# Kernel tuning notes

Hardware: AMD Instinct MI355X
Metric: run time of the kernel (lower is better)

## Reference

```python
import jax, jax.numpy as jnp
import numpy as np

P_TOKENS = 200  # num_prompt_tokens
N_HEADS = 4


def setup_inputs() -> dict:
    key = jax.random.key(0)
    ks = jax.random.split(key, 6)
    B, N, C = 64, 1224, 1024
    D = 256  # bottleneck / down_size
    s = 0.02
    return {
        "x": jax.random.normal(ks[0], (B, N, C), dtype=jnp.float32),
        "down_W": jax.random.normal(ks[1], (D, C), dtype=jnp.float32) * s,
        "down_b": jnp.zeros((D,), jnp.float32),
        "up_W": jax.random.normal(ks[2], (C, D), dtype=jnp.float32) * s,
        "up_b": jnp.zeros((C,), jnp.float32),
        "in_proj_W": jax.random.normal(ks[3], (3 * D, D), dtype=jnp.float32) * s,
        "in_proj_b": jnp.zeros((3 * D,), jnp.float32),
        "out_proj_W": jax.random.normal(ks[4], (D, D), dtype=jnp.float32) * s,
        "out_proj_b": jnp.zeros((D,), jnp.float32),
        "gate": jnp.float32(1.0),
    }


def _forward(x, down_W, down_b, up_W, up_b, in_proj_W, in_proj_b,
             out_proj_W, out_proj_b, gate):
    B, N, C = x.shape
    E = down_W.shape[0]
    hd = E // N_HEADS
    # down projection + exact GELU (torch nn.GELU default)
    down = jax.nn.gelu(x @ down_W.T + down_b, approximate=False)  # [B,N,E]
    prompt = down[:, :P_TOKENS, :]   # [B,P,E]
    tok = down[:, P_TOKENS:, :]      # [B,T,E]
    # --- nn.MultiheadAttention(prompt, prompt, prompt) ---
    qkv = prompt @ in_proj_W.T + in_proj_b            # [B,P,3E]
    q, k, v = jnp.split(qkv, 3, axis=-1)
    def heads(t):
        return t.reshape(B, P_TOKENS, N_HEADS, hd)
    q, k, v = heads(q), heads(k), heads(v)
    attn = jnp.einsum('bqhd,bkhd->bhqk', q, k) / jnp.sqrt(jnp.float32(hd))
    attn = jax.nn.softmax(attn, axis=-1)
    sa = jnp.einsum('bhqk,bkhd->bqhd', attn, v).reshape(B, P_TOKENS, E)
    sa = sa @ out_proj_W.T + out_proj_b               # [B,P,E]
    # --- manual cross attention prompt -> tokens ---
    scale = jnp.float32(E) ** -0.5
    cross = jax.nn.softmax(jnp.einsum('bpe,bte->bpt', sa, tok) * scale, axis=-1)
    prompt_out = jnp.einsum('bpt,bte->bpe', cross, tok)  # [B,P,E]
    combined = jnp.concatenate([prompt_out, tok], axis=1)  # [B,N,E]
    up = combined @ up_W.T + up_b                          # [B,N,C]
    return gate * up


def reference(x, down_W, down_b, up_W, up_b, in_proj_W, in_proj_b,
              out_proj_W, out_proj_b, gate):
    return _forward(x, down_W, down_b, up_W, up_b, in_proj_W, in_proj_b,
                    out_proj_W, out_proj_b, gate)
```

## Files before the change

### kernel.cpp

```cpp
#include <hip/hip_runtime.h>
#include <math.h>

#define BB 64
#define NN 1224
#define CC 1024
#define DD 256
#define PP 200
#define TT 1024
#define HH 4
#define HDD 64

typedef __attribute__((ext_vector_type(8))) short bf16x8;
typedef __attribute__((ext_vector_type(4))) float f32x4;
typedef unsigned short u16;
typedef unsigned long long u64;

__device__ __forceinline__ u16 f2bf(float f) {
  union { float f; unsigned int u; } v; v.f = f;
  unsigned int r = v.u + 0x7FFF + ((v.u >> 16) & 1);
  return (u16)(r >> 16);
}
__device__ __forceinline__ float bf2f(u16 h) {
  union { unsigned int u; float f; } v; v.u = ((unsigned int)h) << 16;
  return v.f;
}
__device__ __forceinline__ unsigned int pk2(float a, float b) {
  return (unsigned int)f2bf(a) | ((unsigned int)f2bf(b) << 16);
}
__device__ __forceinline__ void gload16(const void* g, void* l) {
  __builtin_amdgcn_global_load_lds(
      (const __attribute__((address_space(1))) void*)g,
      (__attribute__((address_space(3))) void*)l, 16, 0, 0);
}

static const size_t SZ_DOWN = (size_t)BB * NN * DD * 2;
static const size_t SZ_TOKT = (size_t)BB * DD * TT * 2;
static const size_t SZ_Q    = (size_t)BB * HH * PP * HDD * 2;
static const size_t SZ_SCORES = (size_t)BB * PP * TT * 2;

static const size_t B_DOWN   = 0;
static const size_t B_TOKT   = B_DOWN + SZ_DOWN;
static const size_t B_POOL   = B_TOKT + SZ_TOKT;
static const size_t B_QB     = B_POOL;
static const size_t B_KB     = B_QB + SZ_Q;
static const size_t B_VB     = B_KB + SZ_Q;
static const size_t B_SA     = B_VB + SZ_Q;
static const size_t B_SA2    = B_SA + SZ_Q;
static const size_t B_PBF    = B_POOL;
static const size_t B_POUTBF = B_SA2;
static const size_t B_SCORES = B_SA2 + SZ_Q;
static const size_t B_W      = B_SCORES + SZ_SCORES * 2;
static const size_t B_WD     = B_W;
static const size_t B_WU     = B_WD + 524288;
static const size_t B_WIP    = B_WU + 524288;
static const size_t B_WOP    = B_WIP + 393216;

#define GEMM_VARS \
  const int tid = threadIdx.x; \
  const int lane = tid & 63, wave = tid >> 6; \
  const int wm = wave >> 2, wn = wave & 3; \
  f32x4 acc[4][4] = {};

#define MFMA_STEP(Ab, Bb) \
  _Pragma("unroll") \
  for (int kk = 0; kk < 64; kk += 32) { \
    bf16x8 af[4], bfr[4]; \
    _Pragma("unroll") \
    for (int mi = 0; mi < 4; ++mi) { \
      const int R = wm * 64 + mi * 16 + (lane & 15); \
      const int byt = (R * 128 + (kk + (lane >> 4) * 8) * 2) ^ ((R & 7) << 4); \
      af[mi] = *(const bf16x8*)((const char*)Ab + byt); \
    } \
    _Pragma("unroll") \
    for (int ni = 0; ni < 4; ++ni) { \
      const int R = wn * 64 + ni * 16 + (lane & 15); \
      const int byt = (R * 128 + (kk + (lane >> 4) * 8) * 2) ^ ((R & 7) << 4); \
      bfr[ni] = *(const bf16x8*)((const char*)Bb + byt); \
    } \
    _Pragma("unroll") \
    for (int mi = 0; mi < 4; ++mi) \
      _Pragma("unroll") \
      for (int ni = 0; ni < 4; ++ni) \
        acc[mi][ni] = __builtin_amdgcn_mfma_f32_16x16x32_bf16(af[mi], bfr[ni], acc[mi][ni], 0, 0, 0); \
  }

#define GLOAD_A2(Ab, SRC) \
  _Pragma("unroll") \
  for (int ii = 0; ii < 2; ++ii) { \
    const int slot = wave * 2 + ii; \
    const int L = slot * 1024 + lane * 16; \
    const int r = L >> 7; \
    const int ce = ((L & 127) ^ ((r & 7) << 4)) >> 1; \
    gload16((SRC), (char*)Ab + slot * 1024); \
  }

#define GLOAD_B4(Bb, SRC) \
  _Pragma("unroll") \
  for (int ii = 0; ii < 4; ++ii) { \
    const int slot = wave * 4 + ii; \
    const int L = slot * 1024 + lane * 16; \
    const int r = L >> 7; \
    const int ce = ((L & 127) ^ ((r & 7) << 4)) >> 1; \
    gload16((SRC), (char*)Bb + slot * 1024); \
  }

#define MFMA_STEP64(Ab, Bb) \
  _Pragma("unroll") \
  for (int kk = 0; kk < 64; kk += 32) { \
    bf16x8 af[4], bfr[2]; \
    _Pragma("unroll") \
    for (int mi = 0; mi < 4; ++mi) { \
      const int R = mi * 16 + (lane & 15); \
      const int byt = (R * 128 + (kk + (lane >> 4) * 8) * 2) ^ ((R & 7) << 4); \
      af[mi] = *(const bf16x8*)((const char*)Ab + byt); \
    } \
    _Pragma("unroll") \
    for (int ni = 0; ni < 2; ++ni) { \
      const int R = wave * 32 + ni * 16 + (lane & 15); \
      const int byt = (R * 128 + (kk + (lane >> 4) * 8) * 2) ^ ((R & 7) << 4); \
      bfr[ni] = *(const bf16x8*)((const char*)Bb + byt); \
    } \
    _Pragma("unroll") \
    for (int mi = 0; mi < 4; ++mi) \
      _Pragma("unroll") \
      for (int ni = 0; ni < 2; ++ni) \
        acc[mi][ni] = __builtin_amdgcn_mfma_f32_16x16x32_bf16(af[mi], bfr[ni], acc[mi][ni], 0, 0, 0); \
  }

#define GLOAD_A1(Ab, SRC) \
  { \
    const int L = wave * 1024 + lane * 16; \
    const int r = L >> 7; \
    const int ce = ((L & 127) ^ ((r & 7) << 4)) >> 1; \
    gload16((SRC), (char*)Ab + wave * 1024); \
  }

__global__ __launch_bounds__(256) void k_castw(const float* __restrict__ dW,
                                               const float* __restrict__ uW,
                                               const float* __restrict__ iW,
                                               const float* __restrict__ oW,
                                               u16* __restrict__ dWb, u16* __restrict__ uWb,
                                               u16* __restrict__ iWb, u16* __restrict__ oWb)
{
  const int id = blockIdx.x * 256 + threadIdx.x;
  const float* s; u16* d; int off;
  if (id < 65536)       { s = dW; d = dWb; off = id; }
  else if (id < 131072) { s = uW; d = uWb; off = id - 65536; }
  else if (id < 180224) { s = iW; d = iWb; off = id - 131072; }
  else                  { s = oW; d = oWb; off = id - 180224; }
  const float4 v = ((const float4*)s)[off];
  uint2 p; p.x = pk2(v.x, v.y); p.y = pk2(v.z, v.w);
  *(uint2*)&d[(size_t)off * 4] = p;
}

__global__ __launch_bounds__(512) void k_down(const float* __restrict__ x,
                                              const u16* __restrict__ Wd,
                                              const float* __restrict__ bias,
                                              u16* __restrict__ out)
{
  __shared__ u16 Ab[2][64 * 64];
  __shared__ u16 Bb[2][256 * 64];
  const int tid = threadIdx.x;
  const int lane = tid & 63, wave = tid >> 6;
  f32x4 acc[4][2] = {};
  const int m0 = blockIdx.x * 64;
  const int ar0 = tid >> 4;
  const int c4 = (tid & 15) * 4;

  float4 areg[2];
#pragma unroll
  for (int i = 0; i < 2; ++i)
    areg[i] = *(const float4*)&x[(size_t)(m0 + ar0 + 32 * i) * CC + c4];
#pragma unroll
  for (int i = 0; i < 2; ++i) {
    const int r = ar0 + 32 * i;
    uint2 p; p.x = pk2(areg[i].x, areg[i].y); p.y = pk2(areg[i].z, areg[i].w);
    *(uint2*)((char*)Ab[0] + ((r * 128 + c4 * 2) ^ ((r & 7) << 4))) = p;
  }
  GLOAD_B4(Bb[0], &Wd[(size_t)r * CC + 0 + ce])
#pragma unroll
  for (int i = 0; i < 2; ++i)
    areg[i] = *(const float4*)&x[(size_t)(m0 + ar0 + 32 * i) * CC + 64 + c4];

  for (int it = 0; it < 16; ++it) {
    const int cur = it & 1;
    if (it < 14) {
#pragma unroll
      for (int i = 0; i < 2; ++i) {
        const int r = ar0 + 32 * i;
        uint2 p; p.x = pk2(areg[i].x, areg[i].y); p.y = pk2(areg[i].z, areg[i].w);
        *(uint2*)((char*)Ab[cur ^ 1] + ((r * 128 + c4 * 2) ^ ((r & 7) << 4))) = p;
      }
      const int kx = (it + 2) * 64;
#pragma unroll
      for (int i = 0; i < 2; ++i)
        areg[i] = *(const float4*)&x[(size_t)(m0 + ar0 + 32 * i) * CC + kx + c4];
      const int kb = (it + 1) * 64;
      GLOAD_B4(Bb[cur ^ 1], &Wd[(size_t)r * CC + kb + ce])
      asm volatile("s_waitcnt vmcnt(6) lgkmcnt(0)" ::: "memory");
    } else if (it == 14) {
#pragma unroll
      for (int i = 0; i < 2; ++i) {
        const int r = ar0 + 32 * i;
        uint2 p; p.x = pk2(areg[i].x, areg[i].y); p.y = pk2(areg[i].z, areg[i].w);
        *(uint2*)((char*)Ab[cur ^ 1] + ((r * 128 + c4 * 2) ^ ((r & 7) << 4))) = p;
      }
      GLOAD_B4(Bb[cur ^ 1], &Wd[(size_t)r * CC + 960 + ce])
      asm volatile("s_waitcnt vmcnt(4) lgkmcnt(0)" ::: "memory");
    } else {
      asm volatile("s_waitcnt vmcnt(0) lgkmcnt(0)" ::: "memory");
    }
    __builtin_amdgcn_s_barrier();
    __builtin_amdgcn_sched_barrier(0);
    MFMA_STEP64(Ab[cur], Bb[cur])
    asm volatile("s_waitcnt lgkmcnt(0)" ::: "memory");
    __builtin_amdgcn_s_barrier();
    __builtin_amdgcn_sched_barrier(0);
  }
#pragma unroll
  for (int mi = 0; mi < 4; ++mi) {
#pragma unroll
    for (int ni = 0; ni < 2; ++ni) {
      const int col = wave * 32 + ni * 16 + (lane & 15);
      const float bv = bias[col];
#pragma unroll
      for (int r = 0; r < 4; ++r) {
        const int row = m0 + mi * 16 + (lane >> 4) * 4 + r;
        float v = acc[mi][ni][r] + bv;
        v = 0.5f * v * (1.f + erff(v * 0.7071067811865475f));
        out[(size_t)row * DD + col] = f2bf(v);
      }
    }
  }
}

__global__ __launch_bounds__(256) void k_tokT(const u16* __restrict__ down,
                                              u16* __restrict__ tokT)
{
  __shared__ u16 Ls[64][68];
  const int b = blockIdx.z;
  const int t0 = blockIdx.x * 64, e0 = blockIdx.y * 64;
  const int tid = threadIdx.x;
#pragma unroll
  for (int it = 0; it < 4; ++it) {
    const int idx = tid + 256 * it;
    const int r = idx >> 4, c4 = (idx & 15) * 4;
    const u64 v = *(const u64*)&down[((size_t)(b * NN + PP + t0 + r)) * DD + e0 + c4];
    *(u64*)&Ls[r][c4] = v;
  }
  __syncthreads();
#pragma unroll
  for (int it = 0; it < 4; ++it) {
    const int idx = tid + 256 * it;
    const int re = idx >> 4, c4 = (idx & 15) * 4;
    u64 pk = (u64)Ls[c4 + 0][re] | ((u64)Ls[c4 + 1][re] << 16) |
             ((u64)Ls[c4 + 2][re] << 32) | ((u64)Ls[c4 + 3][re] << 48);
    *(u64*)&tokT[((size_t)(b * DD + e0 + re)) * TT + t0 + c4] = pk;
  }
}

__global__ __launch_bounds__(512) void k_qkv(const u16* __restrict__ down,
                                             const u16* __restrict__ Wip,
                                             const float* __restrict__ bias,
                                             u16* __restrict__ qb,
                                             u16* __restrict__ kb,
                                             u16* __restrict__ vb)
{
  __shared__ u16 Ab[128 * 64];
  __shared__ u16 Bb[256 * 64];
  GEMM_VARS
  const int m0 = blockIdx.x * 128;
  const int nt = blockIdx.y;

  for (int k0 = 0; k0 < DD; k0 += 64) {
    GLOAD_A2(Ab, ({ const int m = m0 + r; const int b = m / PP; const int p = m - b * PP;
                    &down[((size_t)(b * NN + p)) * DD + k0 + ce]; }))
    GLOAD_B4(Bb, &Wip[(size_t)(nt * 256 + r) * DD + k0 + ce])
    __syncthreads();
    MFMA_STEP(Ab, Bb)
    __syncthreads();
  }
  u16* dst = (nt == 0) ? qb : ((nt == 1) ? kb : vb);
#pragma unroll
  for (int mi = 0; mi < 4; ++mi) {
#pragma unroll
    for (int ni = 0; ni < 4; ++ni) {
      const int n = wn * 64 + ni * 16 + (lane & 15);
      const float bv = bias[nt * 256 + n];
      const int h = n >> 6, dd = n & 63;
#pragma unroll
      for (int r = 0; r < 4; ++r) {
        const int m = m0 + wm * 64 + mi * 16 + (lane >> 4) * 4 + r;
        const int b = m / PP, p = m - b * PP;
        dst[(((size_t)(b * HH + h)) * PP + p) * HDD + dd] = f2bf(acc[mi][ni][r] + bv);
      }
    }
  }
}

__global__ __launch_bounds__(256) void k_attn(const u16* __restrict__ qb,
                                              const u16* __restrict__ kb,
                                              const u16* __restrict__ vb,
                                              u16* __restrict__ sa)
{
  __shared__ u16 Ks[208 * 64];
  __shared__ u16 Vt[64 * 232];
  __shared__ u16 Pb[4 * 16 * 232];
  const int tid = threadIdx.x, lane = tid & 63, wave = tid >> 6;
  const int bh = blockIdx.x;
  const size_t kvbase = (size_t)bh * (PP * HDD);

  for (int it = 0; it < 13; ++it) {
    const int idx = tid + 256 * it;
    if (idx < 3200) {
      const int e = idx * 4;
      const int j = e >> 6, d = e & 63;
      const u64 kv = *(const u64*)&kb[kvbase + e];
      const int byt = (j * 128 + d * 2) ^ ((j & 7) << 4);
      *(u64*)((char*)Ks + byt) = kv;
      const u64 vv = *(const u64*)&vb[kvbase + e];
      const u16* vp = (const u16*)&vv;
#pragma unroll
      for (int w = 0; w < 4; ++w) Vt[(d + w) * 232 + j] = vp[w];
    }
  }
  if (tid < 128) {
    const int rr = 200 + (tid >> 4), c = (tid & 15) * 4;
    const int byt = (rr * 128 + c * 2) ^ ((rr & 7) << 4);
    *(u64*)((char*)Ks + byt) = 0ULL;
  }
#pragma unroll
  for (int w = 0; w < 2; ++w) {
    const int idx = tid + 256 * w;
    const int d = idx >> 3, cg = idx & 7;
    *(u64*)&Vt[d * 232 + 200 + cg * 4] = 0ULL;
  }
  {
    u16* pw = Pb + wave * (16 * 232);
#pragma unroll
    for (int w = 0; w < 2; ++w) {
      const int idx = lane + 64 * w;
      if (idx < 96) {
        const int row = idx / 6, cg = idx - row * 6;
        *(u64*)&pw[row * 232 + 208 + cg * 4] = 0ULL;
      }
    }
  }
  __syncthreads();

  const int b_ = bh >> 2, h = bh & 3;
  const u16* qbase = qb + kvbase;
  u16* pw = Pb + wave * (16 * 232);

  for (int f = wave; f < 13; f += 4) {
    int qrow = f * 16 + (lane & 15); if (qrow > 199) qrow = 199;
    bf16x8 qa[2];
#pragma unroll
    for (int kk = 0; kk < 2; ++kk)
      qa[kk] = *(const bf16x8*)&qbase[(size_t)qrow * 64 + kk * 32 + (lane >> 4) * 8];

    f32x4 s[13];
#pragma unroll
    for (int nf = 0; nf < 13; ++nf) {
      const int R = nf * 16 + (lane & 15);
      f32x4 a = {};
#pragma unroll
      for (int kk = 0; kk < 2; ++kk) {
        const int byt = (R * 128 + (kk * 32 + (lane >> 4) * 8) * 2) ^ ((R & 7) << 4);
        const bf16x8 kf = *(const bf16x8*)((const char*)Ks + byt);
        a = __builtin_amdgcn_mfma_f32_16x16x32_bf16(qa[kk], kf, a, 0, 0, 0);
      }
      s[nf] = a;
    }
    float mx[4] = {-1e30f, -1e30f, -1e30f, -1e30f};
#pragma unroll
    for (int nf = 0; nf < 13; ++nf) {
      const int col = nf * 16 + (lane & 15);
#pragma unroll
      for (int r = 0; r < 4; ++r) {
        float v = (col < PP) ? s[nf][r] * 0.125f : -INFINITY;
        s[nf][r] = v;
        mx[r] = fmaxf(mx[r], v);
      }
    }
#pragma unroll
    for (int off = 1; off < 16; off <<= 1)
#pragma unroll
      for (int r = 0; r < 4; ++r) mx[r] = fmaxf(mx[r], __shfl_xor(mx[r], off));
    float sum[4] = {0.f, 0.f, 0.f, 0.f};
#pragma unroll
    for (int nf = 0; nf < 13; ++nf)
#pragma unroll
      for (int r = 0; r < 4; ++r) {
        const float e = expf(s[nf][r] - mx[r]);
        s[nf][r] = e;
        sum[r] += e;
      }
#pragma unroll
    for (int off = 1; off < 16; off <<= 1)
#pragma unroll
      for (int r = 0; r < 4; ++r) sum[r] += __shfl_xor(sum[r], off);
    float inv[4];
#pragma unroll
    for (int r = 0; r < 4; ++r) inv[r] = 1.f / sum[r];
#pragma unroll
    for (int nf = 0; nf < 13; ++nf) {
      const int col = nf * 16 + (lane & 15);
#pragma unroll
      for (int r = 0; r < 4; ++r) {
        const int row = (lane >> 4) * 4 + r;
        pw[row * 232 + col] = f2bf(s[nf][r] * inv[r]);
      }
    }
    f32x4 o[4] = {};
#pragma unroll
    for (int kk = 0; kk < 7; ++kk) {
      const bf16x8 pa = *(const bf16x8*)((const char*)pw +
                         ((lane & 15) * 232 + kk * 32 + (lane >> 4) * 8) * 2);
#pragma unroll
      for (int nf4 = 0; nf4 < 4; ++nf4) {
        const bf16x8 vv = *(const bf16x8*)((const char*)Vt +
                           (((lane & 15) + 16 * nf4) * 232 + kk * 32 + (lane >> 4) * 8) * 2);
        o[nf4] = __builtin_amdgcn_mfma_f32_16x16x32_bf16(pa, vv, o[nf4], 0, 0, 0);
      }
    }
#pragma unroll
    for (int nf4 = 0; nf4 < 4; ++nf4) {
      const int d = (lane & 15) + 16 * nf4;
#pragma unroll
      for (int r = 0; r < 4; ++r) {
        const int p = f * 16 + (lane >> 4) * 4 + r;
        if (p < PP)
          sa[((size_t)(b_ * PP + p)) * DD + h * HDD + d] = f2bf(o[nf4][r]);
      }
    }
  }
}

__global__ __launch_bounds__(512) void k_oproj(const u16* __restrict__ A,
                                               const u16* __restrict__ Wop,
                                               const float* __restrict__ bias,
                                               u16* __restrict__ out)
{
  __shared__ u16 Ab[128 * 64];
  __shared__ u16 Bb[256 * 64];
  GEMM_VARS
  const int m0 = blockIdx.x * 128;

  for (int k0 = 0; k0 < DD; k0 += 64) {
    GLOAD_A2(Ab, &A[(size_t)(m0 + r) * DD + k0 + ce])
    GLOAD_B4(Bb, &Wop[(size_t)r * DD + k0 + ce])
    __syncthreads();
    MFMA_STEP(Ab, Bb)
    __syncthreads();
  }
#pragma unroll
  for (int mi = 0; mi < 4; ++mi) {
#pragma unroll
    for (int ni = 0; ni < 4; ++ni) {
      const int col = wn * 64 + ni * 16 + (lane & 15);
      const float bv = bias[col];
#pragma unroll
      for (int r = 0; r < 4; ++r) {
        const int row = m0 + wm * 64 + mi * 16 + (lane >> 4) * 4 + r;
        out[(size_t)row * DD + col] = f2bf(acc[mi][ni][r] + bv);
      }
    }
  }
}

__global__ __launch_bounds__(512) void k_scores(const u16* __restrict__ sa2,
                                                const u16* __restrict__ down,
                                                u16* __restrict__ scores)
{
  __shared__ u16 Ab[128 * 64];
  __shared__ u16 Bb[256 * 64];
  GEMM_VARS
  const int b = blockIdx.x, mh = blockIdx.y, nt = blockIdx.z;

  for (int k0 = 0; k0 < DD; k0 += 64) {
    GLOAD_A2(Ab, ({ int p = mh * 128 + r; p = (p < PP) ? p : (PP - 1);
                    &sa2[((size_t)(b * PP + p)) * DD + k0 + ce]; }))
    GLOAD_B4(Bb, &down[((size_t)(b * NN + PP + nt * 256 + r)) * DD + k0 + ce])
    __syncthreads();
    MFMA_STEP(Ab, Bb)
    __syncthreads();
  }
#pragma unroll
  for (int mi = 0; mi < 4; ++mi) {
#pragma unroll
    for (int ni = 0; ni < 4; ++ni) {
      const int t = nt * 256 + wn * 64 + ni * 16 + (lane & 15);
#pragma unroll
      for (int r = 0; r < 4; ++r) {
        const int p = mh * 128 + wm * 64 + mi * 16 + (lane >> 4) * 4 + r;
        if (p < PP)
          scores[((size_t)(b * PP + p)) * TT + t] = f2bf(acc[mi][ni][r] * 0.0625f);
      }
    }
  }
}

__global__ __launch_bounds__(256) void k_softmax(const u16* __restrict__ s,
                                                 u16* __restrict__ pbf)
{
  const int row = blockIdx.x;
  const int t = threadIdx.x;
  const int lane = t & 63, w = t >> 6;
  __shared__ float red[4];
  const u64 raw = *(const u64*)&s[(size_t)row * TT + t * 4];
  float v[4];
#pragma unroll
  for (int i = 0; i < 4; ++i) v[i] = bf2f((u16)(raw >> (16 * i)));
  float mx = fmaxf(fmaxf(v[0], v[1]), fmaxf(v[2], v[3]));
#pragma unroll
  for (int off = 32; off; off >>= 1) mx = fmaxf(mx, __shfl_xor(mx, off));
  if (lane == 0) red[w] = mx;
  __syncthreads();
  mx = fmaxf(fmaxf(red[0], red[1]), fmaxf(red[2], red[3]));
  __syncthreads();
  float sum = 0.f;
#pragma unroll
  for (int i = 0; i < 4; ++i) { v[i] = expf(v[i] - mx); sum += v[i]; }
#pragma unroll
  for (int off = 32; off; off >>= 1) sum += __shfl_xor(sum, off);
  if (lane == 0) red[w] = sum;
  __syncthreads();
  sum = red[0] + red[1] + red[2] + red[3];
  const float inv = 1.f / sum;
  u64 pk = (u64)f2bf(v[0] * inv) | ((u64)f2bf(v[1] * inv) << 16) |
           ((u64)f2bf(v[2] * inv) << 32) | ((u64)f2bf(v[3] * inv) << 48);
  *(u64*)&pbf[(size_t)row * TT + t * 4] = pk;
}

__global__ __launch_bounds__(512) void k_pout(const u16* __restrict__ pbf,
                                              const u16* __restrict__ tokT,
                                              u16* __restrict__ out)
{
  __shared__ u16 Ab[128 * 64];
  __shared__ u16 Bb[256 * 64];
  GEMM_VARS
  const int b = blockIdx.x, mh = blockIdx.y;

  for (int k0 = 0; k0 < TT; k0 += 64) {
    GLOAD_A2(Ab, ({ int p = mh * 128 + r; p = (p < PP) ? p : (PP - 1);
                    &pbf[((size_t)(b * PP + p)) * TT + k0 + ce]; }))
    GLOAD_B4(Bb, &tokT[((size_t)(b * DD + r)) * TT + k0 + ce])
    __syncthreads();
    MFMA_STEP(Ab, Bb)
    __syncthreads();
  }
#pragma unroll
  for (int mi = 0; mi < 4; ++mi) {
#pragma unroll
    for (int ni = 0; ni < 4; ++ni) {
      const int e = wn * 64 + ni * 16 + (lane & 15);
#pragma unroll
      for (int r = 0; r < 4; ++r) {
        const int p = mh * 128 + wm * 64 + mi * 16 + (lane >> 4) * 4 + r;
        if (p < PP)
          out[((size_t)(b * PP + p)) * DD + e] = f2bf(acc[mi][ni][r]);
      }
    }
  }
}

__global__ __launch_bounds__(512) void k_up(const u16* __restrict__ poutbf,
                                            const u16* __restrict__ down,
                                            const u16* __restrict__ Wu,
                                            const float* __restrict__ bias,
                                            const float* __restrict__ gate,
                                            float* __restrict__ out)
{
  __shared__ u16 Ab[2][64 * 64];
  __shared__ u16 Bb[2][256 * 64];
  const int tid = threadIdx.x;
  const int lane = tid & 63, wave = tid >> 6;
  f32x4 acc[4][2] = {};
  const int m0 = blockIdx.x * 64;
  const int n0 = blockIdx.y * 256;

  GLOAD_A1(Ab[0], ({ const int m = m0 + r; const int b = m / NN; const int rr = m - b * NN;
                     const u16* base = (rr < PP) ? &poutbf[((size_t)(b * PP + rr)) * DD]
                                                 : &down[((size_t)(b * NN + rr)) * DD];
                     base + 0 + ce; }))
  GLOAD_B4(Bb[0], &Wu[(size_t)(n0 + r) * DD + 0 + ce])

  for (int it = 0; it < 4; ++it) {
    const int cur = it & 1;
    if (it < 3) {
      const int k0 = (it + 1) * 64;
      GLOAD_A1(Ab[cur ^ 1], ({ const int m = m0 + r; const int b = m / NN; const int rr = m - b * NN;
                               const u16* base = (rr < PP) ? &poutbf[((size_t)(b * PP + rr)) * DD]
                                                           : &down[((size_t)(b * NN + rr)) * DD];
                               base + k0 + ce; }))
      GLOAD_B4(Bb[cur ^ 1], &Wu[(size_t)(n0 + r) * DD + k0 + ce])
      asm volatile("s_waitcnt vmcnt(5)" ::: "memory");
    } else {
      asm volatile("s_waitcnt vmcnt(0)" ::: "memory");
    }
    __builtin_amdgcn_s_barrier();
    __builtin_amdgcn_sched_barrier(0);
    MFMA_STEP64(Ab[cur], Bb[cur])
    asm volatile("s_waitcnt lgkmcnt(0)" ::: "memory");
    __builtin_amdgcn_s_barrier();
    __builtin_amdgcn_sched_barrier(0);
  }
  const float g = gate[0];
#pragma unroll
  for (int mi = 0; mi < 4; ++mi) {
#pragma unroll
    for (int ni = 0; ni < 2; ++ni) {
      const int col = n0 + wave * 32 + ni * 16 + (lane & 15);
      const float bv = bias[col];
#pragma unroll
      for (int r = 0; r < 4; ++r) {
        const int row = m0 + mi * 16 + (lane >> 4) * 4 + r;
        out[(size_t)row * CC + col] = (acc[mi][ni][r] + bv) * g;
      }
    }
  }
}

extern "C" void kernel_launch(void* const* d_in, const int* in_sizes, int n_in,
                              void* d_out, int out_size, void* d_ws, size_t ws_size,
                              hipStream_t stream) {
  const float* x          = (const float*)d_in[0];
  const float* down_W     = (const float*)d_in[1];
  const float* down_b     = (const float*)d_in[2];
  const float* up_W       = (const float*)d_in[3];
  const float* up_b       = (const float*)d_in[4];
  const float* in_proj_W  = (const float*)d_in[5];
  const float* in_proj_b  = (const float*)d_in[6];
  const float* out_proj_W = (const float*)d_in[7];
  const float* out_proj_b = (const float*)d_in[8];
  const float* gate       = (const float*)d_in[9];
  float* out = (float*)d_out;

  char* wsb = (char*)d_ws;
  u16* down_bf = (u16*)(wsb + B_DOWN);
  u16* tokT    = (u16*)(wsb + B_TOKT);
  u16* qb      = (u16*)(wsb + B_QB);
  u16* kb      = (u16*)(wsb + B_KB);
  u16* vb      = (u16*)(wsb + B_VB);
  u16* sa_bf   = (u16*)(wsb + B_SA);
  u16* sa2_bf  = (u16*)(wsb + B_SA2);
  u16* pbf     = (u16*)(wsb + B_PBF);
  u16* poutbf  = (u16*)(wsb + B_POUTBF);
  u16* scores  = (u16*)(wsb + B_SCORES);
  u16* Wd  = (u16*)(wsb + B_WD);
  u16* Wu  = (u16*)(wsb + B_WU);
  u16* Wip = (u16*)(wsb + B_WIP);
  u16* Wop = (u16*)(wsb + B_WOP);

  k_castw<<<dim3(768), 256, 0, stream>>>(down_W, up_W, in_proj_W, out_proj_W, Wd, Wu, Wip, Wop);
  k_down<<<dim3((BB * NN) / 64), 512, 0, stream>>>(x, Wd, down_b, down_bf);
  k_tokT<<<dim3(16, 4, BB), 256, 0, stream>>>(down_bf, tokT);
  k_qkv<<<dim3(100, 3), 512, 0, stream>>>(down_bf, Wip, in_proj_b, qb, kb, vb);
  k_attn<<<dim3(BB * HH), 256, 0, stream>>>(qb, kb, vb, sa_bf);
  k_oproj<<<dim3(100), 512, 0, stream>>>(sa_bf, Wop, out_proj_b, sa2_bf);
  k_scores<<<dim3(BB, 2, 4), 512, 0, stream>>>(sa2_bf, down_bf, scores);
  k_softmax<<<dim3(BB * PP), 256, 0, stream>>>(scores, pbf);
  k_pout<<<dim3(BB, 2), 512, 0, stream>>>(pbf, tokT, poutbf);
  k_up<<<dim3((BB * NN) / 64, CC / 256), 512, 0, stream>>>(poutbf, down_bf, Wu, up_b, gate, out);
}
```

Baseline: 356.3 us.

## Double-buffer small GEMMs with 64-row tiles and use nontemporal loads/stores for x and output

Converts the qkv, oproj, scores and pout GEMM kernels from single-buffered 128x256 tiles with __syncthreads to the double-buffered 64x256 pipeline with async global->LDS loads already used in k_down/k_up, doubling their grid sizes. It also switches k_down's x loads and k_up's output stores to nontemporal. The aim is to overlap load latency with MFMA and raise occupancy on the smaller kernels, and to avoid cache pollution on the streaming tensors. Smaller tiles reduce B-operand reuse per block.

Result: faster. 317.6 us (-10.9%).

```diff
diff --git a/kernel.cpp b/kernel.cpp
--- a/kernel.cpp
+++ b/kernel.cpp
@@ -31,6 +31,9 @@
   __builtin_amdgcn_global_load_lds(
       (const __attribute__((address_space(1))) void*)g,
       (__attribute__((address_space(3))) void*)l, 16, 0, 0);
+}
+__device__ __forceinline__ f32x4 ntld4(const float* p) {
+  return __builtin_nontemporal_load((const f32x4*)p);
 }
 
 static const size_t SZ_DOWN = (size_t)BB * NN * DD * 2;
@@ -54,55 +57,6 @@
 static const size_t B_WU     = B_WD + 524288;
 static const size_t B_WIP    = B_WU + 524288;
 static const size_t B_WOP    = B_WIP + 393216;
-
-#define GEMM_VARS \
-  const int tid = threadIdx.x; \
-  const int lane = tid & 63, wave = tid >> 6; \
-  const int wm = wave >> 2, wn = wave & 3; \
-  f32x4 acc[4][4] = {};
-
-#define MFMA_STEP(Ab, Bb) \
-  _Pragma("unroll") \
-  for (int kk = 0; kk < 64; kk += 32) { \
-    bf16x8 af[4], bfr[4]; \
-    _Pragma("unroll") \
-    for (int mi = 0; mi < 4; ++mi) { \
-      const int R = wm * 64 + mi * 16 + (lane & 15); \
-      const int byt = (R * 128 + (kk + (lane >> 4) * 8) * 2) ^ ((R & 7) << 4); \
-      af[mi] = *(const bf16x8*)((const char*)Ab + byt); \
-    } \
-    _Pragma("unroll") \
-    for (int ni = 0; ni < 4; ++ni) { \
-      const int R = wn * 64 + ni * 16 + (lane & 15); \
-      const int byt = (R * 128 + (kk + (lane >> 4) * 8) * 2) ^ ((R & 7) << 4); \
-      bfr[ni] = *(const bf16x8*)((const char*)Bb + byt); \
-    } \
-    _Pragma("unroll") \
-    for (int mi = 0; mi < 4; ++mi) \
-      _Pragma("unroll") \
-      for (int ni = 0; ni < 4; ++ni) \
-        acc[mi][ni] = __builtin_amdgcn_mfma_f32_16x16x32_bf16(af[mi], bfr[ni], acc[mi][ni], 0, 0, 0); \
-  }
-
-#define GLOAD_A2(Ab, SRC) \
-  _Pragma("unroll") \
-  for (int ii = 0; ii < 2; ++ii) { \
-    const int slot = wave * 2 + ii; \
-    const int L = slot * 1024 + lane * 16; \
-    const int r = L >> 7; \
-    const int ce = ((L & 127) ^ ((r & 7) << 4)) >> 1; \
-    gload16((SRC), (char*)Ab + slot * 1024); \
-  }
-
-#define GLOAD_B4(Bb, SRC) \
-  _Pragma("unroll") \
-  for (int ii = 0; ii < 4; ++ii) { \
-    const int slot = wave * 4 + ii; \
-    const int L = slot * 1024 + lane * 16; \
-    const int r = L >> 7; \
-    const int ce = ((L & 127) ^ ((r & 7) << 4)) >> 1; \
-    gload16((SRC), (char*)Bb + slot * 1024); \
-  }
 
 #define MFMA_STEP64(Ab, Bb) \
   _Pragma("unroll") \
@@ -135,6 +89,25 @@
     gload16((SRC), (char*)Ab + wave * 1024); \
   }
 
+#define GLOAD_B4(Bb, SRC) \
+  _Pragma("unroll") \
+  for (int ii = 0; ii < 4; ++ii) { \
+    const int slot = wave * 4 + ii; \
+    const int L = slot * 1024 + lane * 16; \
+    const int r = L >> 7; \
+    const int ce = ((L & 127) ^ ((r & 7) << 4)) >> 1; \
+    gload16((SRC), (char*)Bb + slot * 1024); \
+  }
+
+#define PIPE_WAIT(N) asm volatile("s_waitcnt vmcnt(" #N ")" ::: "memory");
+#define PIPE_BAR() \
+  __builtin_amdgcn_s_barrier(); \
+  __builtin_amdgcn_sched_barrier(0);
+#define PIPE_END() \
+  asm volatile("s_waitcnt lgkmcnt(0)" ::: "memory"); \
+  __builtin_amdgcn_s_barrier(); \
+  __builtin_amdgcn_sched_barrier(0);
+
 __global__ __launch_bounds__(256) void k_castw(const float* __restrict__ dW,
                                                const float* __restrict__ uW,
                                                const float* __restrict__ iW,
@@ -167,10 +140,10 @@
   const int ar0 = tid >> 4;
   const int c4 = (tid & 15) * 4;
 
-  float4 areg[2];
+  f32x4 areg[2];
 #pragma unroll
   for (int i = 0; i < 2; ++i)
-    areg[i] = *(const float4*)&x[(size_t)(m0 + ar0 + 32 * i) * CC + c4];
+    areg[i] = ntld4(&x[(size_t)(m0 + ar0 + 32 * i) * CC + c4]);
 #pragma unroll
   for (int i = 0; i < 2; ++i) {
     const int r = ar0 + 32 * i;
@@ -180,7 +153,7 @@
   GLOAD_B4(Bb[0], &Wd[(size_t)r * CC + 0 + ce])
 #pragma unroll
   for (int i = 0; i < 2; ++i)
-    areg[i] = *(const float4*)&x[(size_t)(m0 + ar0 + 32 * i) * CC + 64 + c4];
+    areg[i] = ntld4(&x[(size_t)(m0 + ar0 + 32 * i) * CC + 64 + c4]);
 
   for (int it = 0; it < 16; ++it) {
     const int cur = it & 1;
@@ -194,7 +167,7 @@
       const int kx = (it + 2) * 64;
 #pragma unroll
       for (int i = 0; i < 2; ++i)
-        areg[i] = *(const float4*)&x[(size_t)(m0 + ar0 + 32 * i) * CC + kx + c4];
+        areg[i] = ntld4(&x[(size_t)(m0 + ar0 + 32 * i) * CC + kx + c4]);
       const int kb = (it + 1) * 64;
       GLOAD_B4(Bb[cur ^ 1], &Wd[(size_t)r * CC + kb + ce])
       asm volatile("s_waitcnt vmcnt(6) lgkmcnt(0)" ::: "memory");
@@ -210,12 +183,9 @@
     } else {
       asm volatile("s_waitcnt vmcnt(0) lgkmcnt(0)" ::: "memory");
     }
-    __builtin_amdgcn_s_barrier();
-    __builtin_amdgcn_sched_barrier(0);
+    PIPE_BAR()
     MFMA_STEP64(Ab[cur], Bb[cur])
-    asm volatile("s_waitcnt lgkmcnt(0)" ::: "memory");
-    __builtin_amdgcn_s_barrier();
-    __builtin_amdgcn_sched_barrier(0);
+    PIPE_END()
   }
 #pragma unroll
   for (int mi = 0; mi < 4; ++mi) {
@@ -266,31 +236,42 @@
                                              u16* __restrict__ kb,
                                              u16* __restrict__ vb)
 {
-  __shared__ u16 Ab[128 * 64];
-  __shared__ u16 Bb[256 * 64];
-  GEMM_VARS
-  const int m0 = blockIdx.x * 128;
+  __shared__ u16 Ab[2][64 * 64];
+  __shared__ u16 Bb[2][256 * 64];
+  const int tid = threadIdx.x;
+  const int lane = tid & 63, wave = tid >> 6;
+  f32x4 acc[4][2] = {};
+  const int m0 = blockIdx.x * 64;
   const int nt = blockIdx.y;
 
-  for (int k0 = 0; k0 < DD; k0 += 64) {
-    GLOAD_A2(Ab, ({ const int m = m0 + r; const int b = m / PP; const int p = m - b * PP;
-                    &down[((size_t)(b * NN + p)) * DD + k0 + ce]; }))
-    GLOAD_B4(Bb, &Wip[(size_t)(nt * 256 + r) * DD + k0 + ce])
-    __syncthreads();
-    MFMA_STEP(Ab, Bb)
-    __syncthreads();
-  }
+#define QKV_A(BUF, K0) GLOAD_A1(BUF, ({ const int m = m0 + r; const int b = m / PP; const int p = m - b * PP; \
+                    &down[((size_t)(b * NN + p)) * DD + (K0) + ce]; }))
+  QKV_A(Ab[0], 0)
+  GLOAD_B4(Bb[0], &Wip[(size_t)(nt * 256 + r) * DD + 0 + ce])
+  for (int it = 0; it < 4; ++it) {
+    const int cur = it & 1;
+    if (it < 3) {
+      const int k0 = (it + 1) * 64;
+      QKV_A(Ab[cur ^ 1], k0)
+      GLOAD_B4(Bb[cur ^ 1], &Wip[(size_t)(nt * 256 + r) * DD + k0 + ce])
+      PIPE_WAIT(5)
+    } else { PIPE_WAIT(0) }
+    PIPE_BAR()
+    MFMA_STEP64(Ab[cur], Bb[cur])
+    PIPE_END()
+  }
+#undef QKV_A
   u16* dst = (nt == 0) ? qb : ((nt == 1) ? kb : vb);
 #pragma unroll
   for (int mi = 0; mi < 4; ++mi) {
 #pragma unroll
-    for (int ni = 0; ni < 4; ++ni) {
-      const int n = wn * 64 + ni * 16 + (lane & 15);
+    for (int ni = 0; ni < 2; ++ni) {
+      const int n = wave * 32 + ni * 16 + (lane & 15);
       const float bv = bias[nt * 256 + n];
       const int h = n >> 6, dd = n & 63;
 #pragma unroll
       for (int r = 0; r < 4; ++r) {
-        const int m = m0 + wm * 64 + mi * 16 + (lane >> 4) * 4 + r;
+        const int m = m0 + mi * 16 + (lane >> 4) * 4 + r;
         const int b = m / PP, p = m - b * PP;
         dst[(((size_t)(b * HH + h)) * PP + p) * HDD + dd] = f2bf(acc[mi][ni][r] + bv);
       }
@@ -442,27 +423,36 @@
                                                const float* __restrict__ bias,
                                                u16* __restrict__ out)
 {
-  __shared__ u16 Ab[128 * 64];
-  __shared__ u16 Bb[256 * 64];
-  GEMM_VARS
-  const int m0 = blockIdx.x * 128;
-
-  for (int k0 = 0; k0 < DD; k0 += 64) {
-    GLOAD_A2(Ab, &A[(size_t)(m0 + r) * DD + k0 + ce])
-    GLOAD_B4(Bb, &Wop[(size_t)r * DD + k0 + ce])
-    __syncthreads();
-    MFMA_STEP(Ab, Bb)
-    __syncthreads();
+  __shared__ u16 Ab[2][64 * 64];
+  __shared__ u16 Bb[2][256 * 64];
+  const int tid = threadIdx.x;
+  const int lane = tid & 63, wave = tid >> 6;
+  f32x4 acc[4][2] = {};
+  const int m0 = blockIdx.x * 64;
+
+  GLOAD_A1(Ab[0], &A[(size_t)(m0 + r) * DD + 0 + ce])
+  GLOAD_B4(Bb[0], &Wop[(size_t)r * DD + 0 + ce])
+  for (int it = 0; it < 4; ++it) {
+    const int cur = it & 1;
+    if (it < 3) {
+      const int k0 = (it + 1) * 64;
+      GLOAD_A1(Ab[cur ^ 1], &A[(size_t)(m0 + r) * DD + k0 + ce])
+      GLOAD_B4(Bb[cur ^ 1], &Wop[(size_t)r * DD + k0 + ce])
+      PIPE_WAIT(5)
+    } else { PIPE_WAIT(0) }
+    PIPE_BAR()
+    MFMA_STEP64(Ab[cur], Bb[cur])
+    PIPE_END()
   }
 #pragma unroll
   for (int mi = 0; mi < 4; ++mi) {
 #pragma unroll
-    for (int ni = 0; ni < 4; ++ni) {
-      const int col = wn * 64 + ni * 16 + (lane & 15);
+    for (int ni = 0; ni < 2; ++ni) {
+      const int col = wave * 32 + ni * 16 + (lane & 15);
       const float bv = bias[col];
 #pragma unroll
       for (int r = 0; r < 4; ++r) {
-        const int row = m0 + wm * 64 + mi * 16 + (lane >> 4) * 4 + r;
+        const int row = m0 + mi * 16 + (lane >> 4) * 4 + r;
         out[(size_t)row * DD + col] = f2bf(acc[mi][ni][r] + bv);
       }
     }
@@ -473,27 +463,38 @@
                                                 const u16* __restrict__ down,
                                                 u16* __restrict__ scores)
 {
-  __shared__ u16 Ab[128 * 64];
-  __shared__ u16 Bb[256 * 64];
-  GEMM_VARS
+  __shared__ u16 Ab[2][64 * 64];
+  __shared__ u16 Bb[2][256 * 64];
+  const int tid = threadIdx.x;
+  const int lane = tid & 63, wave = tid >> 6;
+  f32x4 acc[4][2] = {};
   const int b = blockIdx.x, mh = blockIdx.y, nt = blockIdx.z;
 
-  for (int k0 = 0; k0 < DD; k0 += 64) {
-    GLOAD_A2(Ab, ({ int p = mh * 128 + r; p = (p < PP) ? p : (PP - 1);
-                    &sa2[((size_t)(b * PP + p)) * DD + k0 + ce]; }))
-    GLOAD_B4(Bb, &down[((size_t)(b * NN + PP + nt * 256 + r)) * DD + k0 + ce])
-    __syncthreads();
-    MFMA_STEP(Ab, Bb)
-    __syncthreads();
-  }
+#define SC_A(BUF, K0) GLOAD_A1(BUF, ({ int p = mh * 64 + r; p = (p < PP) ? p : (PP - 1); \
+                    &sa2[((size_t)(b * PP + p)) * DD + (K0) + ce]; }))
+  SC_A(Ab[0], 0)
+  GLOAD_B4(Bb[0], &down[((size_t)(b * NN + PP + nt * 256 + r)) * DD + 0 + ce])
+  for (int it = 0; it < 4; ++it) {
+    const int cur = it & 1;
+    if (it < 3) {
+      const int k0 = (it + 1) * 64;
+      SC_A(Ab[cur ^ 1], k0)
+      GLOAD_B4(Bb[cur ^ 1], &down[((size_t)(b * NN + PP + nt * 256 + r)) * DD + k0 + ce])
+      PIPE_WAIT(5)
+    } else { PIPE_WAIT(0) }
+    PIPE_BAR()
+    MFMA_STEP64(Ab[cur], Bb[cur])
+    PIPE_END()
+  }
+#undef SC_A
 #pragma unroll
   for (int mi = 0; mi < 4; ++mi) {
 #pragma unroll
-    for (int ni = 0; ni < 4; ++ni) {
-      const int t = nt * 256 + wn * 64 + ni * 16 + (lane & 15);
-#pragma unroll
-      for (int r = 0; r < 4; ++r) {
-        const int p = mh * 128 + wm * 64 + mi * 16 + (lane >> 4) * 4 + r;
+    for (int ni = 0; ni < 2; ++ni) {
+      const int t = nt * 256 + wave * 32 + ni * 16 + (lane & 15);
+#pragma unroll
+      for (int r = 0; r < 4; ++r) {
+        const int p = mh * 64 + mi * 16 + (lane >> 4) * 4 + r;
         if (p < PP)
           scores[((size_t)(b * PP + p)) * TT + t] = f2bf(acc[mi][ni][r] * 0.0625f);
       }
@@ -537,27 +538,38 @@
                                               const u16* __restrict__ tokT,
                                               u16* __restrict__ out)
 {
-  __shared__ u16 Ab[128 * 64];
-  __shared__ u16 Bb[256 * 64];
-  GEMM_VARS
+  __shared__ u16 Ab[2][64 * 64];
+  __shared__ u16 Bb[2][256 * 64];
+  const int tid = threadIdx.x;
+  const int lane = tid & 63, wave = tid >> 6;
+  f32x4 acc[4][2] = {};
   const int b = blockIdx.x, mh = blockIdx.y;
 
-  for (int k0 = 0; k0 < TT; k0 += 64) {
-    GLOAD_A2(Ab, ({ int p = mh * 128 + r; p = (p < PP) ? p : (PP - 1);
-                    &pbf[((size_t)(b * PP + p)) * TT + k0 + ce]; }))
-    GLOAD_B4(Bb, &tokT[((size_t)(b * DD + r)) * TT + k0 + ce])
-    __syncthreads();
-    MFMA_STEP(Ab, Bb)
-    __syncthreads();
-  }
+#define PO_A(BUF, K0) GLOAD_A1(BUF, ({ int p = mh * 64 + r; p = (p < PP) ? p : (PP - 1); \
+                    &pbf[((size_t)(b * PP + p)) * TT + (K0) + ce]; }))
+  PO_A(Ab[0], 0)
+  GLOAD_B4(Bb[0], &tokT[((size_t)(b * DD + r)) * TT + 0 + ce])
+  for (int it = 0; it < 16; ++it) {
+    const int cur = it & 1;
+    if (it < 15) {
+      const int k0 = (it + 1) * 64;
+      PO_A(Ab[cur ^ 1], k0)
+      GLOAD_B4(Bb[cur ^ 1], &tokT[((size_t)(b * DD + r)) * TT + k0 + ce])
+      PIPE_WAIT(5)
+    } else { PIPE_WAIT(0) }
+    PIPE_BAR()
+    MFMA_STEP64(Ab[cur], Bb[cur])
+    PIPE_END()
+  }
+#undef PO_A
 #pragma unroll
   for (int mi = 0; mi < 4; ++mi) {
 #pragma unroll
-    for (int ni = 0; ni < 4; ++ni) {
-      const int e = wn * 64 + ni * 16 + (lane & 15);
-#pragma unroll
-      for (int r = 0; r < 4; ++r) {
-        const int p = mh * 128 + wm * 64 + mi * 16 + (lane >> 4) * 4 + r;
+    for (int ni = 0; ni < 2; ++ni) {
+      const int e = wave * 32 + ni * 16 + (lane & 15);
+#pragma unroll
+      for (int r = 0; r < 4; ++r) {
+        const int p = mh * 64 + mi * 16 + (lane >> 4) * 4 + r;
         if (p < PP)
           out[((size_t)(b * PP + p)) * DD + e] = f2bf(acc[mi][ni][r]);
       }
@@ -580,32 +592,25 @@
   const int m0 = blockIdx.x * 64;
   const int n0 = blockIdx.y * 256;
 
-  GLOAD_A1(Ab[0], ({ const int m = m0 + r; const int b = m / NN; const int rr = m - b * NN;
-                     const u16* base = (rr < PP) ? &poutbf[((size_t)(b * PP + rr)) * DD]
-                                                 : &down[((size_t)(b * NN + rr)) * DD];
-                     base + 0 + ce; }))
+#define UP_A(BUF, K0) GLOAD_A1(BUF, ({ const int m = m0 + r; const int b = m / NN; const int rr = m - b * NN; \
+                     const u16* base = (rr < PP) ? &poutbf[((size_t)(b * PP + rr)) * DD] \
+                                                 : &down[((size_t)(b * NN + rr)) * DD]; \
+                     base + (K0) + ce; }))
+  UP_A(Ab[0], 0)
   GLOAD_B4(Bb[0], &Wu[(size_t)(n0 + r) * DD + 0 + ce])
-
   for (int it = 0; it < 4; ++it) {
     const int cur = it & 1;
     if (it < 3) {
       const int k0 = (it + 1) * 64;
-      GLOAD_A1(Ab[cur ^ 1], ({ const int m = m0 + r; const int b = m / NN; const int rr = m - b * NN;
-                               const u16* base = (rr < PP) ? &poutbf[((size_t)(b * PP + rr)) * DD]
-                                                           : &down[((size_t)(b * NN + rr)) * DD];
-                               base + k0 + ce; }))
+      UP_A(Ab[cur ^ 1], k0)
       GLOAD_B4(Bb[cur ^ 1], &Wu[(size_t)(n0 + r) * DD + k0 + ce])
-      asm volatile("s_waitcnt vmcnt(5)" ::: "memory");
-    } else {
-      asm volatile("s_waitcnt vmcnt(0)" ::: "memory");
-    }
-    __builtin_amdgcn_s_barrier();
-    __builtin_amdgcn_sched_barrier(0);
+      PIPE_WAIT(5)
+    } else { PIPE_WAIT(0) }
+    PIPE_BAR()
     MFMA_STEP64(Ab[cur], Bb[cur])
-    asm volatile("s_waitcnt lgkmcnt(0)" ::: "memory");
-    __builtin_amdgcn_s_barrier();
-    __builtin_amdgcn_sched_barrier(0);
-  }
+    PIPE_END()
+  }
+#undef UP_A
   const float g = gate[0];
 #pragma unroll
   for (int mi = 0; mi < 4; ++mi) {
@@ -616,7 +621,7 @@
 #pragma unroll
       for (int r = 0; r < 4; ++r) {
         const int row = m0 + mi * 16 + (lane >> 4) * 4 + r;
-        out[(size_t)row * CC + col] = (acc[mi][ni][r] + bv) * g;
+        __builtin_nontemporal_store((acc[mi][ni][r] + bv) * g, &out[(size_t)row * CC + col]);
       }
     }
   }
@@ -656,11 +661,11 @@
   k_castw<<<dim3(768), 256, 0, stream>>>(down_W, up_W, in_proj_W, out_proj_W, Wd, Wu, Wip, Wop);
   k_down<<<dim3((BB * NN) / 64), 512, 0, stream>>>(x, Wd, down_b, down_bf);
   k_tokT<<<dim3(16, 4, BB), 256, 0, stream>>>(down_bf, tokT);
-  k_qkv<<<dim3(100, 3), 512, 0, stream>>>(down_bf, Wip, in_proj_b, qb, kb, vb);
+  k_qkv<<<dim3(200, 3), 512, 0, stream>>>(down_bf, Wip, in_proj_b, qb, kb, vb);
   k_attn<<<dim3(BB * HH), 256, 0, stream>>>(qb, kb, vb, sa_bf);
-  k_oproj<<<dim3(100), 512, 0, stream>>>(sa_bf, Wop, out_proj_b, sa2_bf);
-  k_scores<<<dim3(BB, 2, 4), 512, 0, stream>>>(sa2_bf, down_bf, scores);
+  k_oproj<<<dim3(200), 512, 0, stream>>>(sa_bf, Wop, out_proj_b, sa2_bf);
+  k_scores<<<dim3(BB, 4, 4), 512, 0, stream>>>(sa2_bf, down_bf, scores);
   k_softmax<<<dim3(BB * PP), 256, 0, stream>>>(scores, pbf);
-  k_pout<<<dim3(BB, 2), 512, 0, stream>>>(pbf, tokT, poutbf);
+  k_pout<<<dim3(BB, 4), 512, 0, stream>>>(pbf, tokT, poutbf);
   k_up<<<dim3((BB * NN) / 64, CC / 256), 512, 0, stream>>>(poutbf, down_bf, Wu, up_b, gate, out);
 }
```
